# Kernel tuning notes

Measured on AMD Instinct MI355X. Metric: run time of the kernel, lower is better.

The kernel has to match this reference:

```python
import jax, jax.numpy as jnp
import numpy as np

NUM_HEADS = 16

def setup_inputs() -> dict:
    key = jax.random.key(0)
    k1, k2 = jax.random.split(key)
    B, S, E = 4, 2048, 1024
    head_dim = E // NUM_HEADS  # n_qubits = head_dim = 64
    x = jax.random.normal(k1, (B, S, E), dtype=jnp.float32)
    mask = jnp.zeros((B, S, S), dtype=bool)  # no positions masked
    # trainable RX angles, one per wire (torchquantum RX init ~ U(0, 2pi) scaled; use small randn)
    theta = jax.random.normal(k2, (head_dim,), dtype=jnp.float32)
    return {"x": x, "mask": mask, "theta": theta}

def reference(x, mask, theta):
    B, S, E = x.shape
    H = NUM_HEADS
    D = E // H
    # split heads: [B, H, S, D]
    xh = x.reshape(B, S, H, D).transpose(0, 2, 1, 3)
    # quantum projection: RX(x_i) then RX(theta_i) on |0>, measure PauliZ.
    # RX(a)RX(b) = RX(a+b); <Z> after RX(phi)|0> = cos(phi)  =>  cos(x + theta)
    proj = jnp.cos(xh + theta)  # [B, H, S, D]
    # self-attention with q = k = v = proj
    scores = jnp.einsum('bhsd,bhtd->bhst', proj, proj) / jnp.sqrt(jnp.asarray(D, proj.dtype))
    scores = jnp.where(mask[:, None, :, :], jnp.asarray(-1e9, scores.dtype), scores)
    probs = jax.nn.softmax(scores, axis=-1)  # dropout is identity at inference
    attn = jnp.einsum('bhst,bhtd->bhsd', probs, proj)
    # combine heads
    return attn.transpose(0, 2, 1, 3).reshape(B, S, E)
```

## Files before the change

kernel.cpp:

```cpp
#include <hip/hip_runtime.h>


#define B_ 4
#define H_ 16
#define S_ 2048
#define D_ 64
#define E_ 1024
#define LDK 72

typedef unsigned short u16;
typedef unsigned int u32;
using frag  = __attribute__((ext_vector_type(8))) short;
using f32x4 = __attribute__((ext_vector_type(4))) float;

union f32u { float f; u32 i; };

__device__ __forceinline__ u32 pk2r(float a, float b) {
  f32u x, y; x.f = a; y.f = b;
  x.i += 0x8000u; y.i += 0x8000u;
  return __builtin_amdgcn_perm(y.i, x.i, 0x07060302u);
}

__global__ void __launch_bounds__(256, 2)
qattn_mfma(const float* __restrict__ x, const float* __restrict__ theta,
           float* __restrict__ out) {
  const int tid = threadIdx.x;
  const int w   = tid >> 6;
  const int ln  = tid & 63;
  const int l15 = ln & 15;
  const int qd  = ln >> 4;
  const int bh   = blockIdx.x >> 3;
  const int qblk = blockIdx.x & 7;
  const int b = bh >> 4, h = bh & 15;

  __shared__ __align__(16) u16 kt[64 * LDK];
  __shared__ __align__(16) u16 vt[64 * LDK];
  __shared__ __align__(16) u16 pl[4][64 * LDK];
  __shared__ float th[64];
  __shared__ float lsh[4][64];

  if (tid < 64) th[tid] = theta[tid];
  __syncthreads();

  frag qf[4][2];
  {
    const int qrow = qblk * 256 + w * 64;
    #pragma unroll
    for (int nt = 0; nt < 4; nt++) {
      const float* src = x + ((size_t)(b * S_ + qrow + nt * 16 + l15)) * E_ + h * D_ + qd * 8;
      #pragma unroll
      for (int ks = 0; ks < 2; ks++) {
        float4 a = *(const float4*)(src + ks * 32);
        float4 c = *(const float4*)(src + ks * 32 + 4);
        const int d0 = ks * 32 + qd * 8;
        union { u32 u[4]; frag f; } pk;
        pk.u[0] = pk2r(__cosf(a.x + th[d0 + 0]), __cosf(a.y + th[d0 + 1]));
        pk.u[1] = pk2r(__cosf(a.z + th[d0 + 2]), __cosf(a.w + th[d0 + 3]));
        pk.u[2] = pk2r(__cosf(c.x + th[d0 + 4]), __cosf(c.y + th[d0 + 5]));
        pk.u[3] = pk2r(__cosf(c.z + th[d0 + 6]), __cosf(c.w + th[d0 + 7]));
        qf[nt][ks] = pk.f;
      }
    }
  }

  f32x4 o[4][4];
  #pragma unroll
  for (int i = 0; i < 4; i++)
    #pragma unroll
    for (int j = 0; j < 4; j++) o[i][j] = f32x4{0.f, 0.f, 0.f, 0.f};
  float lp[4] = {0.f, 0.f, 0.f, 0.f};

  for (int t = 0; t < S_ / 64; t++) {
    __syncthreads();

    {
      const int j  = tid >> 2;
      const int c0 = (tid & 3) << 4;
      const float* src = x + ((size_t)(b * S_ + t * 64 + j)) * E_ + h * D_ + c0;
      float4 f0 = ((const float4*)src)[0];
      float4 f1 = ((const float4*)src)[1];
      float4 f2 = ((const float4*)src)[2];
      float4 f3 = ((const float4*)src)[3];
      union { u32 u[8]; uint4 v[2]; } pk;
      pk.u[0] = pk2r(__cosf(f0.x + th[c0 + 0]),  __cosf(f0.y + th[c0 + 1]));
      pk.u[1] = pk2r(__cosf(f0.z + th[c0 + 2]),  __cosf(f0.w + th[c0 + 3]));
      pk.u[2] = pk2r(__cosf(f1.x + th[c0 + 4]),  __cosf(f1.y + th[c0 + 5]));
      pk.u[3] = pk2r(__cosf(f1.z + th[c0 + 6]),  __cosf(f1.w + th[c0 + 7]));
      pk.u[4] = pk2r(__cosf(f2.x + th[c0 + 8]),  __cosf(f2.y + th[c0 + 9]));
      pk.u[5] = pk2r(__cosf(f2.z + th[c0 + 10]), __cosf(f2.w + th[c0 + 11]));
      pk.u[6] = pk2r(__cosf(f3.x + th[c0 + 12]), __cosf(f3.y + th[c0 + 13]));
      pk.u[7] = pk2r(__cosf(f3.z + th[c0 + 14]), __cosf(f3.w + th[c0 + 15]));
      uint4* dst = (uint4*)(kt + j * LDK + c0);
      dst[0] = pk.v[0];
      dst[1] = pk.v[1];
    }
    __syncthreads();

    {
      const int d  = tid & 63;
      const int jh = tid >> 6;
      u16 tmp[16];
      #pragma unroll
      for (int jj = 0; jj < 16; jj++) tmp[jj] = kt[(jh * 16 + jj) * LDK + d];
      union { u32 u[8]; uint4 v[2]; } pk;
      #pragma unroll
      for (int i = 0; i < 8; i++) pk.u[i] = (u32)tmp[2 * i] | ((u32)tmp[2 * i + 1] << 16);
      uint4* dst = (uint4*)(vt + d * LDK + jh * 16);
      dst[0] = pk.v[0];
      dst[1] = pk.v[1];
    }

    #pragma unroll
    for (int mt = 0; mt < 4; mt++) {
      const u16* krow = kt + (mt * 16 + l15) * LDK + qd * 8;
      frag a0 = *(const frag*)(krow);
      frag a1 = *(const frag*)(krow + 32);
      #pragma unroll
      for (int nt = 0; nt < 4; nt++) {
        f32x4 s = f32x4{0.f, 0.f, 0.f, 0.f};
        s = __builtin_amdgcn_mfma_f32_16x16x32_bf16(a0, qf[nt][0], s, 0, 0, 0);
        s = __builtin_amdgcn_mfma_f32_16x16x32_bf16(a1, qf[nt][1], s, 0, 0, 0);
        const float e0 = __expf(s[0] * 0.125f);
        const float e1 = __expf(s[1] * 0.125f);
        const float e2 = __expf(s[2] * 0.125f);
        const float e3 = __expf(s[3] * 0.125f);
        lp[nt] += (e0 + e1) + (e2 + e3);
        uint2 pv;
        pv.x = pk2r(e0, e1);
        pv.y = pk2r(e2, e3);
        *(uint2*)(pl[w] + (nt * 16 + l15) * LDK + mt * 16 + qd * 4) = pv;
      }
    }
    __syncthreads();

    #pragma unroll
    for (int ks = 0; ks < 2; ks++) {
      frag vf[4];
      #pragma unroll
      for (int nt = 0; nt < 4; nt++)
        vf[nt] = *(const frag*)(vt + (nt * 16 + l15) * LDK + ks * 32 + qd * 8);
      #pragma unroll
      for (int mt = 0; mt < 4; mt++) {
        frag pf = *(const frag*)(pl[w] + (mt * 16 + l15) * LDK + ks * 32 + qd * 8);
        #pragma unroll
        for (int nt = 0; nt < 4; nt++)
          o[mt][nt] = __builtin_amdgcn_mfma_f32_16x16x32_bf16(pf, vf[nt], o[mt][nt], 0, 0, 0);
      }
    }
  }

  #pragma unroll
  for (int nt = 0; nt < 4; nt++) {
    float v = lp[nt];
    v += __shfl_xor(v, 16, 64);
    v += __shfl_xor(v, 32, 64);
    if (qd == 0) lsh[w][nt * 16 + l15] = v;
  }
  __syncthreads();

  const int qbase = qblk * 256 + w * 64;
  #pragma unroll
  for (int mt = 0; mt < 4; mt++) {
    float rl[4];
    #pragma unroll
    for (int r = 0; r < 4; r++) rl[r] = 1.0f / lsh[w][mt * 16 + qd * 4 + r];
    #pragma unroll
    for (int nt = 0; nt < 4; nt++) {
      f32x4 a = o[mt][nt];
      #pragma unroll
      for (int r = 0; r < 4; r++) {
        const int qrow = qbase + mt * 16 + qd * 4 + r;
        out[((size_t)(b * S_ + qrow)) * E_ + h * D_ + nt * 16 + l15] = a[r] * rl[r];
      }
    }
  }
}

extern "C" void kernel_launch(void* const* d_in, const int* in_sizes, int n_in,
                              void* d_out, int out_size, void* d_ws, size_t ws_size,
                              hipStream_t stream) {
  const float* x     = (const float*)d_in[0];
  const float* theta = (const float*)d_in[2];
  float* out = (float*)d_out;
  qattn_mfma<<<dim3(B_ * H_ * (S_ / 256)), dim3(256), 0, stream>>>(x, theta, out);
}
```

Before: 227.3 us.

## Precompute bf16 projection and transpose in separate kernel, prefetch K/V tiles

Adds a pre-pass kernel that computes cos(x+theta) once per element into bf16 workspace buffers, one row-major and one transposed. The attention kernel then loads ready bf16 K/V tiles with register prefetch of the next tile, which removes the per-block redundant cosine work and the in-LDS transpose, along with one barrier per iteration. It also uses exp2 with a folded scale and computes row sums with an MFMA against a ones vector instead of scalar accumulation. The cost is an extra kernel launch and workspace traffic, and the fast path depends on the workspace being large enough.

```diff
diff --git a/kernel.cpp b/kernel.cpp
--- a/kernel.cpp
+++ b/kernel.cpp
@@ -19,6 +19,179 @@
   f32u x, y; x.f = a; y.f = b;
   x.i += 0x8000u; y.i += 0x8000u;
   return __builtin_amdgcn_perm(y.i, x.i, 0x07060302u);
+}
+
+__global__ void __launch_bounds__(256)
+proj_kernel(const float* __restrict__ x, const float* __restrict__ theta,
+            u16* __restrict__ proj, u16* __restrict__ projT) {
+  const int tid = threadIdx.x;
+  const int bh = blockIdx.x >> 5;
+  const int st = blockIdx.x & 31;
+  const int b = bh >> 4, h = bh & 15;
+
+  __shared__ float th[64];
+  __shared__ u16 tile[64][LDK];
+  if (tid < 64) th[tid] = theta[tid];
+  __syncthreads();
+
+  const int j  = tid >> 2;
+  const int c0 = (tid & 3) << 4;
+  const float* src = x + ((size_t)(b * S_ + st * 64 + j)) * E_ + h * D_ + c0;
+  float4 f0 = ((const float4*)src)[0];
+  float4 f1 = ((const float4*)src)[1];
+  float4 f2 = ((const float4*)src)[2];
+  float4 f3 = ((const float4*)src)[3];
+  union { u32 u[8]; uint4 v[2]; } pk;
+  pk.u[0] = pk2r(__cosf(f0.x + th[c0 + 0]),  __cosf(f0.y + th[c0 + 1]));
+  pk.u[1] = pk2r(__cosf(f0.z + th[c0 + 2]),  __cosf(f0.w + th[c0 + 3]));
+  pk.u[2] = pk2r(__cosf(f1.x + th[c0 + 4]),  __cosf(f1.y + th[c0 + 5]));
+  pk.u[3] = pk2r(__cosf(f1.z + th[c0 + 6]),  __cosf(f1.w + th[c0 + 7]));
+  pk.u[4] = pk2r(__cosf(f2.x + th[c0 + 8]),  __cosf(f2.y + th[c0 + 9]));
+  pk.u[5] = pk2r(__cosf(f2.z + th[c0 + 10]), __cosf(f2.w + th[c0 + 11]));
+  pk.u[6] = pk2r(__cosf(f3.x + th[c0 + 12]), __cosf(f3.y + th[c0 + 13]));
+  pk.u[7] = pk2r(__cosf(f3.z + th[c0 + 14]), __cosf(f3.w + th[c0 + 15]));
+
+  uint4* pd = (uint4*)(proj + ((size_t)bh * S_ + st * 64 + j) * D_ + c0);
+  pd[0] = pk.v[0];
+  pd[1] = pk.v[1];
+  uint4* ld = (uint4*)(&tile[j][c0]);
+  ld[0] = pk.v[0];
+  ld[1] = pk.v[1];
+  __syncthreads();
+
+  const int dr = tid >> 2;
+  const int sc = (tid & 3) << 4;
+  u16 tmp[16];
+  #pragma unroll
+  for (int i = 0; i < 16; i++) tmp[i] = tile[sc + i][dr];
+  union { u32 u[8]; uint4 v[2]; } tk;
+  #pragma unroll
+  for (int i = 0; i < 8; i++) tk.u[i] = (u32)tmp[2 * i] | ((u32)tmp[2 * i + 1] << 16);
+  uint4* td = (uint4*)(projT + ((size_t)bh * D_ + dr) * S_ + st * 64 + sc);
+  td[0] = tk.v[0];
+  td[1] = tk.v[1];
+}
+
+__global__ void __launch_bounds__(256, 2)
+qattn2(const u16* __restrict__ proj, const u16* __restrict__ projT,
+       float* __restrict__ out) {
+  const int tid = threadIdx.x;
+  const int w   = tid >> 6;
+  const int ln  = tid & 63;
+  const int l15 = ln & 15;
+  const int qd  = ln >> 4;
+  const int bh   = blockIdx.x >> 3;
+  const int qblk = blockIdx.x & 7;
+  const int b = bh >> 4, h = bh & 15;
+
+  __shared__ __align__(16) u16 kt[64 * LDK];
+  __shared__ __align__(16) u16 vt[64 * LDK];
+  __shared__ __align__(16) u16 pl[4][64 * LDK];
+
+  frag qf[4][2];
+  const int qrow = qblk * 256 + w * 64;
+  #pragma unroll
+  for (int nt = 0; nt < 4; nt++) {
+    const u16* src = proj + ((size_t)bh * S_ + qrow + nt * 16 + l15) * D_ + qd * 8;
+    qf[nt][0] = *(const frag*)(src);
+    qf[nt][1] = *(const frag*)(src + 32);
+  }
+
+  f32x4 o[4][4];
+  #pragma unroll
+  for (int i = 0; i < 4; i++)
+    #pragma unroll
+    for (int jj = 0; jj < 4; jj++) o[i][jj] = f32x4{0.f, 0.f, 0.f, 0.f};
+  f32x4 ls[4];
+  #pragma unroll
+  for (int i = 0; i < 4; i++) ls[i] = f32x4{0.f, 0.f, 0.f, 0.f};
+
+  frag ones;
+  #pragma unroll
+  for (int i = 0; i < 8; i++) ones[i] = (short)0x3F80;
+
+  const int j  = tid >> 2;
+  const int c0 = (tid & 3) << 4;
+  const u16* kbase = proj  + (size_t)bh * S_ * D_ + (size_t)j * D_ + c0;
+  const u16* vbase = projT + (size_t)bh * D_ * S_ + (size_t)j * S_ + c0;
+  uint4 ka = ((const uint4*)kbase)[0];
+  uint4 kb = ((const uint4*)kbase)[1];
+  uint4 va = ((const uint4*)vbase)[0];
+  uint4 vb = ((const uint4*)vbase)[1];
+
+  const float cexp = 0.18033688011f;
+
+  for (int t = 0; t < S_ / 64; t++) {
+    __syncthreads();
+    *(uint4*)(kt + j * LDK + c0)     = ka;
+    *(uint4*)(kt + j * LDK + c0 + 8) = kb;
+    *(uint4*)(vt + j * LDK + c0)     = va;
+    *(uint4*)(vt + j * LDK + c0 + 8) = vb;
+    __syncthreads();
+
+    if (t < S_ / 64 - 1) {
+      const u16* kn = kbase + (size_t)(t + 1) * 64 * D_;
+      const u16* vn = vbase + (size_t)(t + 1) * 64;
+      ka = ((const uint4*)kn)[0];
+      kb = ((const uint4*)kn)[1];
+      va = ((const uint4*)vn)[0];
+      vb = ((const uint4*)vn)[1];
+    }
+
+    #pragma unroll
+    for (int mt = 0; mt < 4; mt++) {
+      const u16* krow = kt + (mt * 16 + l15) * LDK + qd * 8;
+      frag a0 = *(const frag*)(krow);
+      frag a1 = *(const frag*)(krow + 32);
+      #pragma unroll
+      for (int nt = 0; nt < 4; nt++) {
+        f32x4 s = f32x4{0.f, 0.f, 0.f, 0.f};
+        s = __builtin_amdgcn_mfma_f32_16x16x32_bf16(a0, qf[nt][0], s, 0, 0, 0);
+        s = __builtin_amdgcn_mfma_f32_16x16x32_bf16(a1, qf[nt][1], s, 0, 0, 0);
+        const float e0 = __builtin_amdgcn_exp2f(s[0] * cexp);
+        const float e1 = __builtin_amdgcn_exp2f(s[1] * cexp);
+        const float e2 = __builtin_amdgcn_exp2f(s[2] * cexp);
+        const float e3 = __builtin_amdgcn_exp2f(s[3] * cexp);
+        uint2 pv;
+        pv.x = pk2r(e0, e1);
+        pv.y = pk2r(e2, e3);
+        *(uint2*)(pl[w] + (nt * 16 + l15) * LDK + mt * 16 + qd * 4) = pv;
+      }
+    }
+
+    #pragma unroll
+    for (int ks = 0; ks < 2; ks++) {
+      frag vf[4];
+      #pragma unroll
+      for (int nt = 0; nt < 4; nt++)
+        vf[nt] = *(const frag*)(vt + (nt * 16 + l15) * LDK + ks * 32 + qd * 8);
+      #pragma unroll
+      for (int mt = 0; mt < 4; mt++) {
+        frag pf = *(const frag*)(pl[w] + (mt * 16 + l15) * LDK + ks * 32 + qd * 8);
+        #pragma unroll
+        for (int nt = 0; nt < 4; nt++)
+          o[mt][nt] = __builtin_amdgcn_mfma_f32_16x16x32_bf16(pf, vf[nt], o[mt][nt], 0, 0, 0);
+        ls[mt] = __builtin_amdgcn_mfma_f32_16x16x32_bf16(pf, ones, ls[mt], 0, 0, 0);
+      }
+    }
+  }
+
+  const int qbase = qblk * 256 + w * 64;
+  #pragma unroll
+  for (int mt = 0; mt < 4; mt++) {
+    float rl[4];
+    #pragma unroll
+    for (int r = 0; r < 4; r++) rl[r] = 1.0f / ls[mt][r];
+    #pragma unroll
+    for (int nt = 0; nt < 4; nt++) {
+      f32x4 a = o[mt][nt];
+      #pragma unroll
+      for (int r = 0; r < 4; r++) {
+        const int qr = qbase + mt * 16 + qd * 4 + r;
+        out[((size_t)(b * S_ + qr)) * E_ + h * D_ + nt * 16 + l15] = a[r] * rl[r];
+      }
+    }
+  }
 }
 
 __global__ void __launch_bounds__(256, 2)
@@ -67,12 +240,11 @@
   #pragma unroll
   for (int i = 0; i < 4; i++)
     #pragma unroll
-    for (int j = 0; j < 4; j++) o[i][j] = f32x4{0.f, 0.f, 0.f, 0.f};
+    for (int jj = 0; jj < 4; jj++) o[i][jj] = f32x4{0.f, 0.f, 0.f, 0.f};
   float lp[4] = {0.f, 0.f, 0.f, 0.f};
 
   for (int t = 0; t < S_ / 64; t++) {
     __syncthreads();
-
     {
       const int j  = tid >> 2;
       const int c0 = (tid & 3) << 4;
@@ -95,7 +267,6 @@
       dst[1] = pk.v[1];
     }
     __syncthreads();
-
     {
       const int d  = tid & 63;
       const int jh = tid >> 6;
@@ -169,8 +340,8 @@
       f32x4 a = o[mt][nt];
       #pragma unroll
       for (int r = 0; r < 4; r++) {
-        const int qrow = qbase + mt * 16 + qd * 4 + r;
-        out[((size_t)(b * S_ + qrow)) * E_ + h * D_ + nt * 16 + l15] = a[r] * rl[r];
+        const int qr = qbase + mt * 16 + qd * 4 + r;
+        out[((size_t)(b * S_ + qr)) * E_ + h * D_ + nt * 16 + l15] = a[r] * rl[r];
       }
     }
   }
@@ -182,5 +353,15 @@
   const float* x     = (const float*)d_in[0];
   const float* theta = (const float*)d_in[2];
   float* out = (float*)d_out;
-  qattn_mfma<<<dim3(B_ * H_ * (S_ / 256)), dim3(256), 0, stream>>>(x, theta, out);
-}
+
+  const size_t elems = (size_t)B_ * H_ * S_ * D_;
+  const size_t need  = 2 * elems * sizeof(u16);
+  if (ws_size >= need) {
+    u16* proj  = (u16*)d_ws;
+    u16* projT = proj + elems;
+    proj_kernel<<<dim3(64 * 32), dim3(256), 0, stream>>>(x, theta, proj, projT);
+    qattn2<<<dim3(B_ * H_ * (S_ / 256)), dim3(256), 0, stream>>>(proj, projT, out);
+  } else {
+    qattn_mfma<<<dim3(B_ * H_ * (S_ / 256)), dim3(256), 0, stream>>>(x, theta, out);
+  }
+}
```

Measured after the change: 209.6 us. -7.8%, faster.
